# Performance work log

Measured on AMD Instinct MI355X. Metric: run time of the kernel, lower is better.

Reference implementation:

```python
import jax, jax.numpy as jnp
import numpy as np

N = 3072          # in_features == out_features (CIFAR-10 flat dim)
BATCH = 8192
K_TOP = 16        # K selected pseudo-diagonals
ALPHA_LR = 0.01   # l in the Dykstra soft top-k
NUM_ITER = 50


def sparse_soft_topk_mask_dykstra(alpha, k, l, num_iter=NUM_ITER):
    """Differentiable sparse top-k mask (Sander et al. 2023, p=2):
    Euclidean projection of alpha/l onto the capped simplex
    {m : 0 <= m <= 1, sum(m) = k}, via Dykstra's alternating projections
    (hyperplane sum=k  <->  box [0,1]^n). Returns exact zeros off the top-k.
    """
    z = alpha / l
    n = z.shape[0]

    def body(carry, _):
        x, p, q = carry
        # project x + p onto hyperplane {sum = k}
        y = x + p
        y = y + (k - jnp.sum(y)) / n
        p = x + p - y
        # project y + q onto box [0, 1]^n
        xn = jnp.clip(y + q, 0.0, 1.0)
        q = y + q - xn
        return (xn, p, q), None

    init = (z, jnp.zeros_like(z), jnp.zeros_like(z))
    (x, _, _), _ = jax.lax.scan(body, init, None, length=num_iter)
    return x


def setup_inputs() -> dict:
    key = jax.random.key(0)
    k1, k2, k3 = jax.random.split(key, 3)
    x = jax.random.normal(k1, (BATCH, N), dtype=jnp.float32)
    # kaiming_uniform_(a=sqrt(5)) on (N, N): bound = sqrt(6/((1+5)*N)) = 1/sqrt(N)
    limit = 1.0 / float(np.sqrt(N))
    V = jax.random.uniform(k2, (N, N), jnp.float32, -limit, limit)
    alpha = jax.random.uniform(k3, (N,), jnp.float32)  # alpha >= 0 as asserted
    return {"x": x, "V": V, "alpha": alpha}


def reference(x, V, alpha):
    n = V.shape[0]
    a_topk = sparse_soft_topk_mask_dykstra(alpha, K_TOP, ALPHA_LR)
    # Pseudo-diagonal mask for diag i: ones at (row=(i+c) % n, col=c).
    # matmul(mask_i, diag(V[i])) scales column c by V[i, c], so
    #   W[r, c] = sum_i a_topk[i] * V[i, c] * [r == (i + c) % n]
    # i.e. exactly one i contributes per (r, c): i = (r - c) mod n.
    # a_topk is exactly zero off the top-k, so this gather equals the
    # original loop over nonzero indices without materializing masks.
    r = jnp.arange(n)
    idx = (r[:, None] - r[None, :]) % n          # (in, out) -> source diag i
    W = a_topk[idx] * V[idx, r[None, :]]          # (in, out)
    # F.linear(x, W): x @ W.T, x: (B, out) -> out: (B, in)
    return x @ W.T
```

## Files before the change

kernel.cpp:

```cpp
#include <hip/hip_runtime.h>
#include <hip/hip_bf16.h>
#include <stdint.h>

#define NDIM 3072
#define BATCHN 8192
#define KTOP 16.0f
#define NITER 50

#define BM 256
#define BN 128
#define BK 64
#define NKT (NDIM / BK)
#define A_BYTES 32768
#define B_BYTES 16384
#define BUF_BYTES 49152

typedef __attribute__((ext_vector_type(8))) short short8;
typedef __attribute__((ext_vector_type(4))) float floatx4;
typedef __attribute__((ext_vector_type(4))) unsigned short ushortx4;

__device__ inline unsigned short f2bf(float f) {
    __hip_bfloat16 h = __float2bfloat16(f);
    return *reinterpret_cast<unsigned short*>(&h);
}

__global__ void dykstra_kernel(const float* __restrict__ alpha, float* __restrict__ a_out) {
    const int lane = threadIdx.x;
    float z[48];
#pragma unroll
    for (int e = 0; e < 48; ++e) z[e] = alpha[e * 64 + lane] / 0.01f;
    float S = 0.f;
#pragma unroll
    for (int e = 0; e < 48; ++e) S += z[e];
#pragma unroll
    for (int m = 1; m < 64; m <<= 1) S += __shfl_xor(S, m, 64);

    float D = 0.f;
    for (int it = 0; it < NITER; ++it) {
        D += (KTOP - S) / (float)NDIM;
        float s2 = 0.f;
#pragma unroll
        for (int e = 0; e < 48; ++e) {
            float v = z[e] + D;
            v = v < 0.f ? 0.f : (v > 1.f ? 1.f : v);
            s2 += v;
        }
        S = s2;
#pragma unroll
        for (int m = 1; m < 64; m <<= 1) S += __shfl_xor(S, m, 64);
    }
#pragma unroll
    for (int e = 0; e < 48; ++e) {
        float v = z[e] + D;
        v = v < 0.f ? 0.f : (v > 1.f ? 1.f : v);
        a_out[e * 64 + lane] = v;
    }
}

__global__ __launch_bounds__(256) void build_w(const float* __restrict__ V,
                                               const float* __restrict__ a,
                                               unsigned short* __restrict__ W) {
    __shared__ float Vs[128][64];
    __shared__ float as_[128];
    const int tid = threadIdx.x;
    const int c0 = blockIdx.x * 64;
    const int r0 = blockIdx.y * 64;
    int ib = r0 - c0 - 63;
    ib %= NDIM; if (ib < 0) ib += NDIM;

    if (tid < 128) {
        int i = ib + tid; if (i >= NDIM) i -= NDIM;
        as_[tid] = a[i];
    }
#pragma unroll
    for (int it = 0; it < 8; ++it) {
        int idx = it * 256 + tid;
        int d = idx >> 4;
        int c4 = (idx & 15) * 4;
        int i = ib + d; if (i >= NDIM) i -= NDIM;
        *(floatx4*)&Vs[d][c4] = *(const floatx4*)&V[(size_t)i * NDIM + c0 + c4];
    }
    __syncthreads();

    const int c4 = (tid & 15) * 4;
    const int rr0 = tid >> 4;
#pragma unroll
    for (int p = 0; p < 4; ++p) {
        int rr = p * 16 + rr0;
        ushortx4 o;
#pragma unroll
        for (int j = 0; j < 4; ++j) {
            int cc = c4 + j;
            int d = rr - cc + 63;
            o[j] = f2bf(as_[d] * Vs[d][cc]);
        }
        *(ushortx4*)&W[(size_t)(r0 + rr) * NDIM + (c0 + c4)] = o;
    }
}

__global__ void convert_x(const float* __restrict__ x, unsigned short* __restrict__ xb, int n) {
    int i = (blockIdx.x * blockDim.x + threadIdx.x) * 4;
    const int stride = gridDim.x * blockDim.x * 4;
    for (; i < n; i += stride) {
        floatx4 v = *(const floatx4*)(x + i);
        ushortx4 o;
        o[0] = f2bf(v[0]); o[1] = f2bf(v[1]); o[2] = f2bf(v[2]); o[3] = f2bf(v[3]);
        *(ushortx4*)(xb + i) = o;
    }
}

__global__ __launch_bounds__(512, 2) void gemm_bt(const unsigned short* __restrict__ A,
                                                  const unsigned short* __restrict__ B,
                                                  float* __restrict__ C) {
    __shared__ __align__(16) char lds[3 * BUF_BYTES];

    const int bid = blockIdx.x;
    const int swz = (bid & 7) * 96 + (bid >> 3);
    const int tm = swz / 24, tn = swz % 24;
    const int m0 = tm * BM, n0 = tn * BN;

    const int tid = threadIdx.x;
    const int lane = tid & 63;
    const int wid = tid >> 6;
    const int wm = wid >> 1;
    const int wn = wid & 1;

    const unsigned short* Ab = A + (size_t)m0 * NDIM;
    const unsigned short* Bb = B + (size_t)n0 * NDIM;

    auto stageA = [&](char* sw, int kt, int i) {
        int c = wid * 4 + i;
        int b = c >> 1, kk = c & 1;
        const unsigned short* g = Ab + (size_t)(b * 16 + (lane & 15)) * NDIM + kt + kk * 32 + (lane >> 4) * 8;
        __builtin_amdgcn_global_load_lds(
            (const __attribute__((address_space(1))) unsigned int*)g,
            (__attribute__((address_space(3))) unsigned int*)(sw + c * 1024 + lane * 16),
            16, 0, 0);
    };
    auto stageB = [&](char* sw, int kt, int i) {
        int c = wid * 2 + i;
        int b = c >> 1, kk = c & 1;
        const unsigned short* g = Bb + (size_t)(b * 16 + (lane & 15)) * NDIM + kt + kk * 32 + (lane >> 4) * 8;
        __builtin_amdgcn_global_load_lds(
            (const __attribute__((address_space(1))) unsigned int*)g,
            (__attribute__((address_space(3))) unsigned int*)(sw + A_BYTES + c * 1024 + lane * 16),
            16, 0, 0);
    };

    floatx4 acc[4][4];
#pragma unroll
    for (int i = 0; i < 4; ++i)
#pragma unroll
        for (int j = 0; j < 4; ++j) acc[i][j] = {0.f, 0.f, 0.f, 0.f};

    {
        char* s0 = lds;
        char* s1 = lds + BUF_BYTES;
#pragma unroll
        for (int i = 0; i < 4; ++i) stageA(s0, 0, i);
        stageB(s0, 0, 0); stageB(s0, 0, 1);
#pragma unroll
        for (int i = 0; i < 4; ++i) stageA(s1, BK, i);
        stageB(s1, BK, 0); stageB(s1, BK, 1);
        asm volatile("s_waitcnt vmcnt(6)" ::: "memory");
        asm volatile("s_barrier" ::: "memory");
    }

    int rb = 0;
    for (int t = 0; t < NKT; ++t) {
        const char* sb = lds + rb * BUF_BYTES;
        int wbi = rb - 1; if (wbi < 0) wbi += 3;
        char* sw = lds + wbi * BUF_BYTES;
        const int kt2 = (t + 2) * BK;
        const bool do_stage = (t + 2) < NKT;

        short8 af[4][2], bf[2][2];
#pragma unroll
        for (int m = 0; m < 4; ++m)
#pragma unroll
            for (int kk = 0; kk < 2; ++kk)
                af[m][kk] = *(const short8*)(sb + (wm * 4 + m) * 2048 + kk * 1024 + lane * 16);
#pragma unroll
        for (int n = 0; n < 2; ++n)
#pragma unroll
            for (int kk = 0; kk < 2; ++kk)
                bf[n][kk] = *(const short8*)(sb + A_BYTES + (wn * 4 + n) * 2048 + kk * 1024 + lane * 16);
        if (do_stage) { stageA(sw, kt2, 0); stageA(sw, kt2, 1); stageA(sw, kt2, 2); }
        asm volatile("s_barrier" ::: "memory");
        __builtin_amdgcn_s_setprio(1);
#pragma unroll
        for (int m = 0; m < 4; ++m)
#pragma unroll
            for (int n = 0; n < 2; ++n)
#pragma unroll
                for (int kk = 0; kk < 2; ++kk)
                    acc[m][n] = __builtin_amdgcn_mfma_f32_16x16x32_bf16(af[m][kk], bf[n][kk], acc[m][n], 0, 0, 0);
        __builtin_amdgcn_s_setprio(0);
        asm volatile("s_barrier" ::: "memory");

        short8 bg[2][2];
#pragma unroll
        for (int n = 0; n < 2; ++n)
#pragma unroll
            for (int kk = 0; kk < 2; ++kk)
                bg[n][kk] = *(const short8*)(sb + A_BYTES + (wn * 4 + 2 + n) * 2048 + kk * 1024 + lane * 16);
        if (do_stage) { stageA(sw, kt2, 3); stageB(sw, kt2, 0); stageB(sw, kt2, 1); }
        asm volatile("s_barrier" ::: "memory");
        __builtin_amdgcn_s_setprio(1);
#pragma unroll
        for (int m = 0; m < 4; ++m)
#pragma unroll
            for (int n = 0; n < 2; ++n)
#pragma unroll
                for (int kk = 0; kk < 2; ++kk)
                    acc[m][2 + n] = __builtin_amdgcn_mfma_f32_16x16x32_bf16(af[m][kk], bg[n][kk], acc[m][2 + n], 0, 0, 0);
        __builtin_amdgcn_s_setprio(0);
        if (t + 2 < NKT)      { asm volatile("s_waitcnt vmcnt(6)" ::: "memory"); }
        else if (t + 1 < NKT) { asm volatile("s_waitcnt vmcnt(0)" ::: "memory"); }
        asm volatile("s_barrier" ::: "memory");

        rb = rb + 1; if (rb == 3) rb = 0;
    }

#pragma unroll
    for (int m = 0; m < 4; ++m)
#pragma unroll
        for (int n = 0; n < 4; ++n)
#pragma unroll
            for (int rg = 0; rg < 4; ++rg) {
                int rr = m0 + wm * 64 + m * 16 + (lane >> 4) * 4 + rg;
                int cc = n0 + wn * 64 + n * 16 + (lane & 15);
                C[(size_t)rr * NDIM + cc] = acc[m][n][rg];
            }
}

extern "C" void kernel_launch(void* const* d_in, const int* in_sizes, int n_in,
                              void* d_out, int out_size, void* d_ws, size_t ws_size,
                              hipStream_t stream) {
    const float* x     = (const float*)d_in[0];
    const float* V     = (const float*)d_in[1];
    const float* alpha = (const float*)d_in[2];
    float* out = (float*)d_out;

    float* a_ws = (float*)d_ws;
    unsigned short* xb = (unsigned short*)((char*)d_ws + 16384);
    unsigned short* Wb = (unsigned short*)((char*)d_ws + 16384 + (size_t)BATCHN * NDIM * 2);

    hipLaunchKernelGGL(dykstra_kernel, dim3(1), dim3(64), 0, stream, alpha, a_ws);
    hipLaunchKernelGGL(build_w, dim3(NDIM / 64, NDIM / 64), dim3(256), 0, stream, V, a_ws, Wb);
    hipLaunchKernelGGL(convert_x, dim3(2048), dim3(256), 0, stream, x, xb, BATCHN * NDIM);
    hipLaunchKernelGGL(gemm_bt, dim3((BATCHN / BM) * (NDIM / BN)), dim3(512), 0, stream,
                       xb, Wb, out);
}
```

Baseline: 455.4 us.

## Double-buffer register fragments and cut per-tile barriers in GEMM main loop

Restructures the bf16 MFMA main loop so the LDS fragments for the next K-tile are read into a second register set while the current tile's 32 MFMAs run. Each tile now has one barrier instead of three, and each wave loads all four B fragments at once rather than two halves. The three LDS buffers are rotated by pointer swapping, and the loop is unrolled by two so the register sets alternate. The aim is to hide LDS read latency and cut synchronisation overhead, at the cost of higher VGPR pressure that could lower occupancy.

```diff
diff --git a/kernel.cpp b/kernel.cpp
--- a/kernel.cpp
+++ b/kernel.cpp
@@ -12,7 +12,6 @@
 #define BK 64
 #define NKT (NDIM / BK)
 #define A_BYTES 32768
-#define B_BYTES 16384
 #define BUF_BYTES 49152
 
 typedef __attribute__((ext_vector_type(8))) short short8;
@@ -147,80 +146,70 @@
             16, 0, 0);
     };
 
+#define STAGE_TILE(SW, KT)  do { \
+        stageA(SW, KT, 0); stageA(SW, KT, 1); stageA(SW, KT, 2); stageA(SW, KT, 3); \
+        stageB(SW, KT, 0); stageB(SW, KT, 1); } while (0)
+
+#define READ_FRAGS(AF, BF, SB)  do { \
+        _Pragma("unroll") \
+        for (int m_ = 0; m_ < 4; ++m_) \
+            _Pragma("unroll") \
+            for (int kk_ = 0; kk_ < 2; ++kk_) \
+                AF[m_][kk_] = *(const short8*)((SB) + (wm * 4 + m_) * 2048 + kk_ * 1024 + lane * 16); \
+        _Pragma("unroll") \
+        for (int n_ = 0; n_ < 4; ++n_) \
+            _Pragma("unroll") \
+            for (int kk_ = 0; kk_ < 2; ++kk_) \
+                BF[n_][kk_] = *(const short8*)((SB) + A_BYTES + (wn * 4 + n_) * 2048 + kk_ * 1024 + lane * 16); } while (0)
+
+#define MFMA_CLUSTER(AF, BF)  do { \
+        __builtin_amdgcn_s_setprio(1); \
+        _Pragma("unroll") \
+        for (int kk_ = 0; kk_ < 2; ++kk_) \
+            _Pragma("unroll") \
+            for (int m_ = 0; m_ < 4; ++m_) \
+                _Pragma("unroll") \
+                for (int n_ = 0; n_ < 4; ++n_) \
+                    acc[m_][n_] = __builtin_amdgcn_mfma_f32_16x16x32_bf16(AF[m_][kk_], BF[n_][kk_], acc[m_][n_], 0, 0, 0); \
+        __builtin_amdgcn_s_setprio(0); } while (0)
+
+#define TILE_BODY(T, AF_CUR, BF_CUR, AF_NXT, BF_NXT)  do { \
+        MFMA_CLUSTER(AF_CUR, BF_CUR); \
+        if ((T) + 2 < NKT) { STAGE_TILE(stg, ((T) + 2) * BK); } \
+        if ((T) + 2 < NKT)      { asm volatile("s_waitcnt vmcnt(6)" ::: "memory"); } \
+        else if ((T) + 1 < NKT) { asm volatile("s_waitcnt vmcnt(0)" ::: "memory"); } \
+        asm volatile("s_barrier" ::: "memory"); \
+        if ((T) + 1 < NKT) { READ_FRAGS(AF_NXT, BF_NXT, nxt); } \
+        char* tmp_ = cur; cur = nxt; nxt = stg; stg = tmp_; } while (0)
+
     floatx4 acc[4][4];
 #pragma unroll
     for (int i = 0; i < 4; ++i)
 #pragma unroll
         for (int j = 0; j < 4; ++j) acc[i][j] = {0.f, 0.f, 0.f, 0.f};
 
-    {
-        char* s0 = lds;
-        char* s1 = lds + BUF_BYTES;
-#pragma unroll
-        for (int i = 0; i < 4; ++i) stageA(s0, 0, i);
-        stageB(s0, 0, 0); stageB(s0, 0, 1);
-#pragma unroll
-        for (int i = 0; i < 4; ++i) stageA(s1, BK, i);
-        stageB(s1, BK, 0); stageB(s1, BK, 1);
-        asm volatile("s_waitcnt vmcnt(6)" ::: "memory");
-        asm volatile("s_barrier" ::: "memory");
-    }
-
-    int rb = 0;
-    for (int t = 0; t < NKT; ++t) {
-        const char* sb = lds + rb * BUF_BYTES;
-        int wbi = rb - 1; if (wbi < 0) wbi += 3;
-        char* sw = lds + wbi * BUF_BYTES;
-        const int kt2 = (t + 2) * BK;
-        const bool do_stage = (t + 2) < NKT;
-
-        short8 af[4][2], bf[2][2];
-#pragma unroll
-        for (int m = 0; m < 4; ++m)
-#pragma unroll
-            for (int kk = 0; kk < 2; ++kk)
-                af[m][kk] = *(const short8*)(sb + (wm * 4 + m) * 2048 + kk * 1024 + lane * 16);
-#pragma unroll
-        for (int n = 0; n < 2; ++n)
-#pragma unroll
-            for (int kk = 0; kk < 2; ++kk)
-                bf[n][kk] = *(const short8*)(sb + A_BYTES + (wn * 4 + n) * 2048 + kk * 1024 + lane * 16);
-        if (do_stage) { stageA(sw, kt2, 0); stageA(sw, kt2, 1); stageA(sw, kt2, 2); }
-        asm volatile("s_barrier" ::: "memory");
-        __builtin_amdgcn_s_setprio(1);
-#pragma unroll
-        for (int m = 0; m < 4; ++m)
-#pragma unroll
-            for (int n = 0; n < 2; ++n)
-#pragma unroll
-                for (int kk = 0; kk < 2; ++kk)
-                    acc[m][n] = __builtin_amdgcn_mfma_f32_16x16x32_bf16(af[m][kk], bf[n][kk], acc[m][n], 0, 0, 0);
-        __builtin_amdgcn_s_setprio(0);
-        asm volatile("s_barrier" ::: "memory");
-
-        short8 bg[2][2];
-#pragma unroll
-        for (int n = 0; n < 2; ++n)
-#pragma unroll
-            for (int kk = 0; kk < 2; ++kk)
-                bg[n][kk] = *(const short8*)(sb + A_BYTES + (wn * 4 + 2 + n) * 2048 + kk * 1024 + lane * 16);
-        if (do_stage) { stageA(sw, kt2, 3); stageB(sw, kt2, 0); stageB(sw, kt2, 1); }
-        asm volatile("s_barrier" ::: "memory");
-        __builtin_amdgcn_s_setprio(1);
-#pragma unroll
-        for (int m = 0; m < 4; ++m)
-#pragma unroll
-            for (int n = 0; n < 2; ++n)
-#pragma unroll
-                for (int kk = 0; kk < 2; ++kk)
-                    acc[m][2 + n] = __builtin_amdgcn_mfma_f32_16x16x32_bf16(af[m][kk], bg[n][kk], acc[m][2 + n], 0, 0, 0);
-        __builtin_amdgcn_s_setprio(0);
-        if (t + 2 < NKT)      { asm volatile("s_waitcnt vmcnt(6)" ::: "memory"); }
-        else if (t + 1 < NKT) { asm volatile("s_waitcnt vmcnt(0)" ::: "memory"); }
-        asm volatile("s_barrier" ::: "memory");
-
-        rb = rb + 1; if (rb == 3) rb = 0;
-    }
+    short8 afP[4][2], bfP[4][2], afQ[4][2], bfQ[4][2];
+
+    char* cur = lds;
+    char* nxt = lds + BUF_BYTES;
+    char* stg = lds + 2 * BUF_BYTES;
+
+    STAGE_TILE(cur, 0);
+    STAGE_TILE(nxt, BK);
+    asm volatile("s_waitcnt vmcnt(6)" ::: "memory");
+    asm volatile("s_barrier" ::: "memory");
+    READ_FRAGS(afP, bfP, cur);
+
+    for (int it = 0; it < NKT / 2; ++it) {
+        const int t0 = 2 * it;
+        TILE_BODY(t0,     afP, bfP, afQ, bfQ);
+        TILE_BODY(t0 + 1, afQ, bfQ, afP, bfP);
+    }
+
+#undef TILE_BODY
+#undef MFMA_CLUSTER
+#undef READ_FRAGS
+#undef STAGE_TILE
 
 #pragma unroll
     for (int m = 0; m < 4; ++m)
```

New measurement: 453.0 us. Within noise of the previous version (-0.5%).
